# Kernel optimization log

Hardware: AMD Instinct MI355X
Metric: run time of the kernel (lower is better)

## Reference

```python
import jax, jax.numpy as jnp
import numpy as np

B, S, D = 4, 2048, 1024
H, DK, DV = 16, 64, 64
SCALE = 8.0  # scaling_factor = sqrt(dk)


def setup_inputs() -> dict:
    key = jax.random.key(0)
    ks = jax.random.split(key, 9)
    s = 1.0 / np.sqrt(D)
    return {
        "q": jax.random.normal(ks[0], (B, S, D), jnp.float32),
        "k": jax.random.normal(ks[1], (B, S, D), jnp.float32),
        "v": jax.random.normal(ks[2], (B, S, D), jnp.float32),
        "Wq": jax.random.uniform(ks[3], (D, H * DK), jnp.float32, -s, s),
        "bq": jax.random.uniform(ks[4], (H * DK,), jnp.float32, -s, s),
        "Wk": jax.random.uniform(ks[5], (D, H * DK), jnp.float32, -s, s),
        "bk": jax.random.uniform(ks[6], (H * DK,), jnp.float32, -s, s),
        "Wv": jax.random.uniform(ks[7], (D, H * DV), jnp.float32, -s, s),
        "bv": jax.random.uniform(ks[8], (H * DV,), jnp.float32, -s, s),
    }


def reference(q, k, v, Wq, bq, Wk, bk, Wv, bv):
    # Linear projections, then split heads: [B,S,H*d] -> [B,S,H,d]
    qh = (q @ Wq + bq).reshape(B, S, H, DK)
    kh = (k @ Wk + bk).reshape(B, S, H, DK)
    vh = (v @ Wv + bv).reshape(B, S, H, DV)
    # scores: [B,H,Sq,Sk]
    e = jnp.einsum("bqhd,bkhd->bhqk", qh, kh) / SCALE
    attn = jax.nn.softmax(e, axis=-1)
    out = jnp.einsum("bhqk,bkhd->bqhd", attn, vh)  # [B,Sq,H,DV]
    return out.reshape(B, S, H * DV)  # dropout p=0 -> identity
```

## Files before the change

### kernel.cpp

```cpp
#include <hip/hip_runtime.h>
#include <hip/hip_bf16.h>


typedef unsigned short u16;
typedef unsigned int   u32;
typedef short bf16x8 __attribute__((ext_vector_type(8)));
typedef short bf16x4 __attribute__((ext_vector_type(4)));
typedef float f32x4  __attribute__((ext_vector_type(4)));
typedef u32   u32x4  __attribute__((ext_vector_type(4)));

#define S_TOT 2048
#define HD    1024
#define QK_SCALE 0.18033688f

#if __has_builtin(__builtin_amdgcn_exp2f)
#define EXP2(x) __builtin_amdgcn_exp2f(x)
#else
#define EXP2(x) exp2f(x)
#endif

__device__ __forceinline__ u16 f2bf(float f) {
  union { float f; unsigned u; } v; v.f = f;
  unsigned r = v.u + 0x7FFFu + ((v.u >> 16) & 1u);
  return (u16)(r >> 16);
}

__device__ __forceinline__ u32 cvt_pk_bf16(float lo, float hi) {
  u32 r;
  asm("v_cvt_pk_bf16_f32 %0, %1, %2" : "=v"(r) : "v"(lo), "v"(hi));
  return r;
}

__device__ __forceinline__ bf16x4 ds_tr16(unsigned a) {
  bf16x4 d;
  asm volatile("ds_read_b64_tr_b16 %0, %1" : "=v"(d) : "v"(a) : "memory");
  return d;
}

__device__ __forceinline__ void gld16(const u16* g, u16* l) {
  __builtin_amdgcn_global_load_lds(
      (const __attribute__((address_space(1))) u32*)g,
      (__attribute__((address_space(3))) u32*)l, 16, 0, 0);
}

#define LGKM_FENCE() do { asm volatile("s_waitcnt lgkmcnt(0)" ::: "memory"); \
                          __builtin_amdgcn_sched_barrier(0); } while (0)

#define PIPE_BAR(N) do { asm volatile("s_waitcnt vmcnt(" #N ")" ::: "memory"); \
                         __builtin_amdgcn_s_barrier(); \
                         __builtin_amdgcn_sched_barrier(0); } while (0)

__global__ __launch_bounds__(256)
void conv_kernel(const float* __restrict__ x0, const float* __restrict__ x1, const float* __restrict__ x2,
                 const float* __restrict__ w0, const float* __restrict__ w1, const float* __restrict__ w2,
                 u16* __restrict__ Xb, u16* __restrict__ Wt)
{
  const int z = blockIdx.y;
  const int t = threadIdx.x;
  if (blockIdx.x < 1024) {
    const float* X = z == 0 ? x0 : (z == 1 ? x1 : x2);
    u16* Xz = Xb + (size_t)z * 8388608;
    int tid = blockIdx.x * 256 + t;
#pragma unroll
    for (int i = 0; i < 8; ++i) {
      int c = tid + i * 262144;
      int row = c >> 8, k4 = (c & 255) * 4;
      const float4 xv = *(const float4*)&X[(size_t)row * 1024 + k4];
      int p = (k4 & ~31) + 8 * ((k4 & 15) >> 2) + 4 * ((k4 >> 4) & 1);
      p ^= (row & 6) << 2;
      bf16x4 sv = { (short)f2bf(xv.x), (short)f2bf(xv.y), (short)f2bf(xv.z), (short)f2bf(xv.w) };
      *(bf16x4*)&Xz[(size_t)row * 1024 + p] = sv;
    }
  } else {
    const float* W = z == 0 ? w0 : (z == 1 ? w1 : w2);
    u16* Wz = Wt + (size_t)z * 1048576;
    int tid = (blockIdx.x - 1024) * 256 + t;
#pragma unroll
    for (int i = 0; i < 8; ++i) {
      int c = tid + i * 32768;
      int n = c & 1023, k4 = (c >> 10) * 4;
      float wv0 = W[(size_t)(k4 + 0) * 1024 + n];
      float wv1 = W[(size_t)(k4 + 1) * 1024 + n];
      float wv2 = W[(size_t)(k4 + 2) * 1024 + n];
      float wv3 = W[(size_t)(k4 + 3) * 1024 + n];
      int kl = k4 & 31;
      int kp = 8 * ((kl & 15) >> 2) + 4 * ((kl >> 4) & 1);
      int off = ((n >> 7) * 32 + (k4 >> 5)) * 4096 + (n & 127) * 32 + kp;
      bf16x4 sv = { (short)f2bf(wv0), (short)f2bf(wv1), (short)f2bf(wv2), (short)f2bf(wv3) };
      *(bf16x4*)&Wz[off] = sv;
    }
  }
}

__global__ __launch_bounds__(256)
void gemm_kernel(const u16* __restrict__ Xb, const u16* __restrict__ Wt,
                 const float* __restrict__ b0, const float* __restrict__ b1, const float* __restrict__ b2,
                 u16* __restrict__ o0, u16* __restrict__ o1, u16* __restrict__ vT)
{
  int p  = blockIdx.x + 8 * blockIdx.y + 512 * blockIdx.z;
  int wk = (p & 7) * 192 + (p >> 3);
  int nb = wk & 7, mb = (wk >> 3) & 63, z = wk >> 9;

  const u16* Xz = Xb + (size_t)z * 8388608;
  const u16* Wz = Wt + (size_t)z * 1048576;
  const float* BS = z == 0 ? b0 : (z == 1 ? b1 : b2);
  const float  osc = (z == 0) ? QK_SCALE : 1.0f;

  const int t = threadIdx.x;
  const int lane = t & 63, wid = t >> 6;
  const int g = lane >> 4, ln = lane & 15;
  const int mbase = mb * 128, nbase = nb * 128;
  const int xr = (ln & 6) << 2;

  __shared__ __align__(16) u16 Al[3][128 * 32];

  f32x4 acc[4][4];
#pragma unroll
  for (int i = 0; i < 4; ++i)
#pragma unroll
    for (int j = 0; j < 4; ++j) { acc[i][j][0]=0.f; acc[i][j][1]=0.f; acc[i][j][2]=0.f; acc[i][j][3]=0.f; }

  const u16* sa = Xz + (size_t)(mbase + (t >> 2)) * 1024 + (t & 3) * 8;
  u16* alw[3] = { &Al[0][wid * 512], &Al[1][wid * 512], &Al[2][wid * 512] };

  auto stage = [&](int kb, int buf) __attribute__((always_inline)) {
    gld16(sa + kb * 32,               alw[buf]);
    gld16(sa + kb * 32 + 64 * 1024,   alw[buf] + 2048);
  };

  const int whalf = (z < 2) ? (wid & 1) : (wid & 1);
  const u16* wfp = Wz + (size_t)(nb * 32) * 4096
                 + (whalf * 64 + ln) * 32 + g * 8;

  auto loadB = [&](int kb, bf16x8* dst) __attribute__((always_inline)) {
#pragma unroll
    for (int nf = 0; nf < 4; ++nf)
      dst[nf] = *(const bf16x8*)(wfp + (size_t)kb * 4096 + nf * 512);
  };

  bf16x8 bA[4], bB[4];

  stage(0, 0);
  loadB(0, bA);
  stage(1, 1);
  PIPE_BAR(6);

  if (z < 2) {
    const int wm = wid >> 1;
    u16* O = z == 0 ? o0 : o1;

    auto compute = [&](int cur, const bf16x8* bq) __attribute__((always_inline)) {
      bf16x8 af[4];
#pragma unroll
      for (int mf = 0; mf < 4; ++mf)
        af[mf] = *(const bf16x8*)&Al[cur][(wm * 64 + mf * 16 + ln) * 32 + (g * 8 ^ xr)];
      __builtin_amdgcn_s_setprio(1);
#pragma unroll
      for (int mf = 0; mf < 4; ++mf)
#pragma unroll
        for (int nf = 0; nf < 4; ++nf)
          acc[mf][nf] = __builtin_amdgcn_mfma_f32_16x16x32_bf16(af[mf], bq[nf], acc[mf][nf], 0, 0, 0);
      __builtin_amdgcn_s_setprio(0);
    };

    for (int kb = 0; kb < 30; kb += 6) {
      stage(kb + 2, 2); loadB(kb + 1, bB); compute(0, bA); PIPE_BAR(6);
      stage(kb + 3, 0); loadB(kb + 2, bA); compute(1, bB); PIPE_BAR(6);
      stage(kb + 4, 1); loadB(kb + 3, bB); compute(2, bA); PIPE_BAR(6);
      stage(kb + 5, 2); loadB(kb + 4, bA); compute(0, bB); PIPE_BAR(6);
      stage(kb + 6, 0); loadB(kb + 5, bB); compute(1, bA); PIPE_BAR(6);
      stage(kb + 7, 1); loadB(kb + 6, bA); compute(2, bB); PIPE_BAR(6);
    }
    loadB(31, bB); compute(0, bA); PIPE_BAR(0);
    compute(1, bB);

#pragma unroll
    for (int nf = 0; nf < 4; ++nf) {
      int n = nbase + whalf * 64 + nf * 16 + ln;
      float bv = BS[n];
#pragma unroll
      for (int mf = 0; mf < 4; ++mf)
#pragma unroll
        for (int r = 0; r < 4; ++r) {
          int m = mbase + wm * 64 + mf * 16 + 4 * g + r;
          O[(size_t)m * 1024 + n] = f2bf((acc[mf][nf][r] + bv) * osc);
        }
    }
  } else {
    const int wseq = wid >> 1;

    auto compute2 = [&](int cur, const bf16x8* wq) __attribute__((always_inline)) {
      bf16x8 bfx[4];
#pragma unroll
      for (int nf = 0; nf < 4; ++nf)
        bfx[nf] = *(const bf16x8*)&Al[cur][(wseq * 64 + nf * 16 + ln) * 32 + (g * 8 ^ xr)];
      __builtin_amdgcn_s_setprio(1);
#pragma unroll
      for (int mf = 0; mf < 4; ++mf)
#pragma unroll
        for (int nf = 0; nf < 4; ++nf)
          acc[mf][nf] = __builtin_amdgcn_mfma_f32_16x16x32_bf16(wq[mf], bfx[nf], acc[mf][nf], 0, 0, 0);
      __builtin_amdgcn_s_setprio(0);
    };

    for (int kb = 0; kb < 30; kb += 6) {
      stage(kb + 2, 2); loadB(kb + 1, bB); compute2(0, bA); PIPE_BAR(6);
      stage(kb + 3, 0); loadB(kb + 2, bA); compute2(1, bB); PIPE_BAR(6);
      stage(kb + 4, 1); loadB(kb + 3, bB); compute2(2, bA); PIPE_BAR(6);
      stage(kb + 5, 2); loadB(kb + 4, bA); compute2(0, bB); PIPE_BAR(6);
      stage(kb + 6, 0); loadB(kb + 5, bB); compute2(1, bA); PIPE_BAR(6);
      stage(kb + 7, 1); loadB(kb + 6, bA); compute2(2, bB); PIPE_BAR(6);
    }
    loadB(31, bB); compute2(0, bA); PIPE_BAR(0);
    compute2(1, bB);

#pragma unroll
    for (int mf = 0; mf < 4; ++mf)
#pragma unroll
      for (int r = 0; r < 4; ++r) {
        int dvg = nbase + whalf * 64 + mf * 16 + 4 * g + r;
        float bv = BS[dvg];
        int hh = dvg >> 6, dvl = dvg & 63;
#pragma unroll
        for (int nf = 0; nf < 4; ++nf) {
          int m = mbase + wseq * 64 + nf * 16 + ln;
          int bb = m >> 11, ss = m & 2047;
          vT[((size_t)(bb * 16 + hh) * 64 + dvl) * 2048 + ss] = f2bf(acc[mf][nf][r] + bv);
        }
      }
  }
}

__global__ __launch_bounds__(256)
void proj_kernel(const float* __restrict__ x0, const float* __restrict__ x1, const float* __restrict__ x2,
                 const float* __restrict__ w0, const float* __restrict__ w1, const float* __restrict__ w2,
                 const float* __restrict__ b0, const float* __restrict__ b1, const float* __restrict__ b2,
                 u16* __restrict__ o0, u16* __restrict__ o1, u16* __restrict__ vT)
{
  int p  = blockIdx.x + 8 * blockIdx.y + 512 * blockIdx.z;
  int wk = (p & 7) * 192 + (p >> 3);
  int nb = wk & 7, mb = (wk >> 3) & 63, z = wk >> 9;

  const float* X  = z == 0 ? x0 : (z == 1 ? x1 : x2);
  const float* W  = z == 0 ? w0 : (z == 1 ? w1 : w2);
  const float* BS = z == 0 ? b0 : (z == 1 ? b1 : b2);
  const float  osc = (z == 0) ? QK_SCALE : 1.0f;

  const int t = threadIdx.x;
  const int lane = t & 63, wid = t >> 6;
  const int g = lane >> 4, ln = lane & 15;
  const int wm = wid >> 1, wn = wid & 1;
  const int mbase = mb * 128, nbase = nb * 128;

  __shared__ __align__(16) u16 As[128 * 40];
  __shared__ __align__(16) u16 Bs[16 * 272];

  f32x4 acc[4][4];
#pragma unroll
  for (int i = 0; i < 4; ++i)
#pragma unroll
    for (int j = 0; j < 4; ++j) { acc[i][j][0]=0.f; acc[i][j][1]=0.f; acc[i][j][2]=0.f; acc[i][j][3]=0.f; }

  const int arow = t >> 3;
  const int ak0  = (t & 7) * 4;
  const int ap   = 8 * ((ak0 & 15) >> 2) + 4 * (ak0 >> 4);
  const int bkr  = t >> 5;
  const int bnc  = (t & 31) * 4;
  const int bnblk = bnc >> 4, bncl = bnc & 15;

  const unsigned bs_base = (unsigned)(size_t)&Bs[0];

  for (int kb = 0; kb < 32; ++kb) {
    const int kbase = kb * 32;
#pragma unroll
    for (int ps = 0; ps < 4; ++ps) {
      int row = arow + 32 * ps;
      const float4 xv = *(const float4*)&X[(size_t)(mbase + row) * 1024 + kbase + ak0];
      bf16x4 sv = { (short)f2bf(xv.x), (short)f2bf(xv.y), (short)f2bf(xv.z), (short)f2bf(xv.w) };
      *(bf16x4*)&As[row * 40 + ap] = sv;
    }
#pragma unroll
    for (int ps = 0; ps < 4; ++ps) {
      int kr = bkr + 8 * ps;
      const float4 wv = *(const float4*)&W[(size_t)(kbase + kr) * 1024 + nbase + bnc];
      bf16x4 sv = { (short)f2bf(wv.x), (short)f2bf(wv.y), (short)f2bf(wv.z), (short)f2bf(wv.w) };
      *(bf16x4*)&Bs[(bnblk * 2 + (kr >> 4)) * 272 + (kr & 15) * 16 + bncl] = sv;
    }
    __syncthreads();

    bf16x8 af[4];
#pragma unroll
    for (int mf = 0; mf < 4; ++mf)
      af[mf] = *(const bf16x8*)&As[(wm * 64 + mf * 16 + ln) * 40 + g * 8];

    bf16x8 bfv[4];
#pragma unroll
    for (int nf = 0; nf < 4; ++nf) {
      unsigned base = bs_base + (unsigned)(((wn * 4 + nf) * 2) * 544) + lane * 8;
      bf16x4 lo = ds_tr16(base);
      bf16x4 hi = ds_tr16(base + 544);
      bf16x8 bb;
      bb[0]=lo[0]; bb[1]=lo[1]; bb[2]=lo[2]; bb[3]=lo[3];
      bb[4]=hi[0]; bb[5]=hi[1]; bb[6]=hi[2]; bb[7]=hi[3];
      bfv[nf] = bb;
    }
    LGKM_FENCE();
#pragma unroll
    for (int mf = 0; mf < 4; ++mf)
#pragma unroll
      for (int nf = 0; nf < 4; ++nf)
        acc[mf][nf] = __builtin_amdgcn_mfma_f32_16x16x32_bf16(af[mf], bfv[nf], acc[mf][nf], 0, 0, 0);
    __syncthreads();
  }

#pragma unroll
  for (int nf = 0; nf < 4; ++nf) {
    int n = nbase + wn * 64 + nf * 16 + ln;
    float bv = BS[n];
#pragma unroll
    for (int mf = 0; mf < 4; ++mf)
#pragma unroll
      for (int r = 0; r < 4; ++r) {
        int m = mbase + wm * 64 + mf * 16 + 4 * g + r;
        float val = (acc[mf][nf][r] + bv) * osc;
        if (z < 2) {
          u16* O = z == 0 ? o0 : o1;
          O[(size_t)m * 1024 + n] = f2bf(val);
        } else {
          vT[((size_t)((m >> 11) * 16 + (n >> 6)) * 64 + (n & 63)) * 2048 + (m & 2047)] = f2bf(val);
        }
      }
  }
}

__global__ __launch_bounds__(512)
void attn_kernel(const u16* __restrict__ qh, const u16* __restrict__ kh, const u16* __restrict__ vT,
                 float* __restrict__ out)
{
  int p  = blockIdx.x + 8 * blockIdx.y + 128 * blockIdx.z;
  int wk = (p & 7) * 64 + (p >> 3);
  int qt = wk & 7, h = (wk >> 3) & 15, b = wk >> 7;

  const int t = threadIdx.x;
  const int lane = t & 63, wid = t >> 6;
  const int g = lane >> 4, ln = lane & 15;
  const size_t bS = (size_t)b * S_TOT;
  const int qwin = qt * 256 + wid * 32;

  __shared__ __align__(16) u16 Ks[64 * 72];
  __shared__ __align__(16) u16 Vt[64 * 72];

  bf16x8 qf[2][2];
#pragma unroll
  for (int nf = 0; nf < 2; ++nf) {
    const u16* qrow = &qh[(bS + qwin + nf * 16 + ln) * HD + h * 64];
#pragma unroll
    for (int kk = 0; kk < 2; ++kk) {
      bf16x4 lo = *(const bf16x4*)&qrow[kk * 32 + 4 * g];
      bf16x4 hi = *(const bf16x4*)&qrow[kk * 32 + 4 * g + 16];
      bf16x8 qq;
      qq[0]=lo[0]; qq[1]=lo[1]; qq[2]=lo[2]; qq[3]=lo[3];
      qq[4]=hi[0]; qq[5]=hi[1]; qq[6]=hi[2]; qq[7]=hi[3];
      qf[nf][kk] = qq;
    }
  }

  bf16x8 ones;
#pragma unroll
  for (int j = 0; j < 8; ++j) ones[j] = (short)0x3F80;

  f32x4 o[2][4];
#pragma unroll
  for (int i = 0; i < 2; ++i)
#pragma unroll
    for (int j = 0; j < 4; ++j) { o[i][j][0]=0.f; o[i][j][1]=0.f; o[i][j][2]=0.f; o[i][j][3]=0.f; }
  f32x4 o1[2];
  o1[0][0]=0.f; o1[0][1]=0.f; o1[0][2]=0.f; o1[0][3]=0.f;
  o1[1][0]=0.f; o1[1][1]=0.f; o1[1][2]=0.f; o1[1][3]=0.f;

  const int skv = t >> 4;
  const int sd0 = (t & 15) * 4;
  const int kpos = 32 * (sd0 >> 5) + 8 * ((sd0 & 15) >> 2) + 4 * ((sd0 >> 4) & 1);
  u16* ksw[2];
  ksw[0] = &Ks[skv * 72 + kpos];
  ksw[1] = &Ks[(skv + 32) * 72 + kpos];
  const u16* kp = &kh[(bS + skv) * HD + h * 64 + sd0];

  const int vdv  = t >> 3;
  const int vkv8 = (t & 7) * 8;
  const int vp0  = 32 * (vkv8 >> 5) + 8 * ((vkv8 & 15) >> 2) + 4 * ((vkv8 >> 4) & 1);
  const int vkv4 = vkv8 + 4;
  const int vp1  = 32 * (vkv4 >> 5) + 8 * ((vkv4 & 15) >> 2) + 4 * ((vkv4 >> 4) & 1);
  u16* vsw0 = &Vt[vdv * 72 + vp0];
  u16* vsw1 = &Vt[vdv * 72 + vp1];
  const u16* vp = &vT[((size_t)(b * 16 + h) * 64 + vdv) * 2048 + vkv8];

  const size_t KSTEP = (size_t)64 * HD, C32 = (size_t)32 * HD;

  bf16x4 kr[2];
  kr[0] = *(const bf16x4*)kp; kr[1] = *(const bf16x4*)(kp + C32);
  bf16x8 vr = *(const bf16x8*)vp;
  kp += KSTEP; vp += 64;

  for (int it = 0; it < 32; ++it) {
    *(bf16x4*)ksw[0] = kr[0];
    *(bf16x4*)ksw[1] = kr[1];
    bf16x4 vlo = { vr[0], vr[1], vr[2], vr[3] };
    bf16x4 vhi = { vr[4], vr[5], vr[6], vr[7] };
    *(bf16x4*)vsw0 = vlo;
    *(bf16x4*)vsw1 = vhi;
    __syncthreads();

    if (it < 31) {
      kr[0] = *(const bf16x4*)kp; kr[1] = *(const bf16x4*)(kp + C32);
      vr = *(const bf16x8*)vp;
      kp += KSTEP; vp += 64;
    }

#pragma unroll
    for (int s = 0; s < 2; ++s) {
      bf16x8 kf[2][2];
#pragma unroll
      for (int mf = 0; mf < 2; ++mf)
#pragma unroll
        for (int kk = 0; kk < 2; ++kk)
          kf[mf][kk] = *(const bf16x8*)&Ks[(s * 32 + mf * 16 + ln) * 72 + kk * 32 + 8 * g];

      f32x4 sc[2][2];
      __builtin_amdgcn_s_setprio(1);
#pragma unroll
      for (int mf = 0; mf < 2; ++mf)
#pragma unroll
        for (int nf = 0; nf < 2; ++nf) {
          f32x4 a; a[0]=0.f; a[1]=0.f; a[2]=0.f; a[3]=0.f;
#pragma unroll
          for (int kk = 0; kk < 2; ++kk)
            a = __builtin_amdgcn_mfma_f32_16x16x32_bf16(kf[mf][kk], qf[nf][kk], a, 0, 0, 0);
          sc[mf][nf] = a;
        }
      __builtin_amdgcn_s_setprio(0);

      bf16x8 vf[4];
#pragma unroll
      for (int nf = 0; nf < 4; ++nf)
        vf[nf] = *(const bf16x8*)&Vt[(nf * 16 + ln) * 72 + s * 32 + 8 * g];

      bf16x8 pa[2];
#pragma unroll
      for (int nf = 0; nf < 2; ++nf) {
        float pv[2][4];
#pragma unroll
        for (int mf = 0; mf < 2; ++mf)
#pragma unroll
          for (int r = 0; r < 4; ++r)
            pv[mf][r] = EXP2(sc[mf][nf][r]);
        union { u32x4 u; bf16x8 b; } pk;
        pk.u[0] = cvt_pk_bf16(pv[0][0], pv[0][1]);
        pk.u[1] = cvt_pk_bf16(pv[0][2], pv[0][3]);
        pk.u[2] = cvt_pk_bf16(pv[1][0], pv[1][1]);
        pk.u[3] = cvt_pk_bf16(pv[1][2], pv[1][3]);
        pa[nf] = pk.b;
      }

      __builtin_amdgcn_s_setprio(1);
#pragma unroll
      for (int mq = 0; mq < 2; ++mq) {
#pragma unroll
        for (int nf = 0; nf < 4; ++nf)
          o[mq][nf] = __builtin_amdgcn_mfma_f32_16x16x32_bf16(pa[mq], vf[nf], o[mq][nf], 0, 0, 0);
        o1[mq] = __builtin_amdgcn_mfma_f32_16x16x32_bf16(pa[mq], ones, o1[mq], 0, 0, 0);
      }
      __builtin_amdgcn_s_setprio(0);
    }
    __syncthreads();
  }

#pragma unroll
  for (int mq = 0; mq < 2; ++mq)
#pragma unroll
    for (int r = 0; r < 4; ++r) {
      float inv = 1.0f / o1[mq][r];
      int qrow = qwin + mq * 16 + 4 * g + r;
#pragma unroll
      for (int nf = 0; nf < 4; ++nf)
        out[(bS + qrow) * HD + h * 64 + nf * 16 + ln] = o[mq][nf][r] * inv;
    }
}

extern "C" void kernel_launch(void* const* d_in, const int* in_sizes, int n_in,
                              void* d_out, int out_size, void* d_ws, size_t ws_size,
                              hipStream_t stream) {
  const float* q  = (const float*)d_in[0];
  const float* k  = (const float*)d_in[1];
  const float* v  = (const float*)d_in[2];
  const float* Wq = (const float*)d_in[3];
  const float* bq = (const float*)d_in[4];
  const float* Wk = (const float*)d_in[5];
  const float* bk = (const float*)d_in[6];
  const float* Wv = (const float*)d_in[7];
  const float* bv = (const float*)d_in[8];
  float* out = (float*)d_out;

  u16* qh = (u16*)d_ws;
  u16* kh = qh + (size_t)8192 * 1024;
  u16* vT = kh + (size_t)8192 * 1024;

  const size_t XB_OFF = (size_t)3 * 8192 * 1024;
  const size_t WT_OFF = XB_OFF + (size_t)3 * 8192 * 1024;
  const size_t NEED   = (WT_OFF + (size_t)3 * 1024 * 1024) * 2;

  if (ws_size >= NEED) {
    u16* Xb = (u16*)d_ws + XB_OFF;
    u16* Wt = (u16*)d_ws + WT_OFF;
    conv_kernel<<<dim3(1152, 3), 256, 0, stream>>>(q, k, v, Wq, Wk, Wv, Xb, Wt);
    gemm_kernel<<<dim3(8, 64, 3), 256, 0, stream>>>(Xb, Wt, bq, bk, bv, qh, kh, vT);
  } else {
    proj_kernel<<<dim3(8, 64, 3), 256, 0, stream>>>(q, k, v, Wq, Wk, Wv, bq, bk, bv, qh, kh, vT);
  }
  attn_kernel<<<dim3(8, 16, 4), 512, 0, stream>>>(qh, kh, vT, out);
}
```

Before: 168.6 us.

## Enlarge projection GEMM tile to 256 rows with 512 threads and 4-stage LDS pipeline

Result: slower. 183.0 us (+8.5%).

```diff
diff --git a/kernel.cpp b/kernel.cpp
--- a/kernel.cpp
+++ b/kernel.cpp
@@ -92,14 +92,14 @@
   }
 }
 
-__global__ __launch_bounds__(256)
+__global__ __launch_bounds__(512)
 void gemm_kernel(const u16* __restrict__ Xb, const u16* __restrict__ Wt,
                  const float* __restrict__ b0, const float* __restrict__ b1, const float* __restrict__ b2,
                  u16* __restrict__ o0, u16* __restrict__ o1, u16* __restrict__ vT)
 {
-  int p  = blockIdx.x + 8 * blockIdx.y + 512 * blockIdx.z;
-  int wk = (p & 7) * 192 + (p >> 3);
-  int nb = wk & 7, mb = (wk >> 3) & 63, z = wk >> 9;
+  int p  = blockIdx.x + 8 * blockIdx.y + 256 * blockIdx.z;
+  int wk = (p & 7) * 96 + (p >> 3);
+  int nb = wk & 7, mb = (wk >> 3) & 31, z = wk >> 8;
 
   const u16* Xz = Xb + (size_t)z * 8388608;
   const u16* Wz = Wt + (size_t)z * 1048576;
@@ -109,10 +109,12 @@
   const int t = threadIdx.x;
   const int lane = t & 63, wid = t >> 6;
   const int g = lane >> 4, ln = lane & 15;
-  const int mbase = mb * 128, nbase = nb * 128;
+  const int wm = wid >> 1;
+  const int whalf = wid & 1;
+  const int mbase = mb * 256, nbase = nb * 128;
   const int xr = (ln & 6) << 2;
 
-  __shared__ __align__(16) u16 Al[3][128 * 32];
+  __shared__ __align__(16) u16 Al[4][256 * 32];
 
   f32x4 acc[4][4];
 #pragma unroll
@@ -121,17 +123,14 @@
     for (int j = 0; j < 4; ++j) { acc[i][j][0]=0.f; acc[i][j][1]=0.f; acc[i][j][2]=0.f; acc[i][j][3]=0.f; }
 
   const u16* sa = Xz + (size_t)(mbase + (t >> 2)) * 1024 + (t & 3) * 8;
-  u16* alw[3] = { &Al[0][wid * 512], &Al[1][wid * 512], &Al[2][wid * 512] };
+  u16* alw[4] = { &Al[0][wid * 512], &Al[1][wid * 512], &Al[2][wid * 512], &Al[3][wid * 512] };
 
   auto stage = [&](int kb, int buf) __attribute__((always_inline)) {
-    gld16(sa + kb * 32,               alw[buf]);
-    gld16(sa + kb * 32 + 64 * 1024,   alw[buf] + 2048);
+    gld16(sa + kb * 32,                alw[buf]);
+    gld16(sa + kb * 32 + 128 * 1024,   alw[buf] + 4096);
   };
 
-  const int whalf = (z < 2) ? (wid & 1) : (wid & 1);
-  const u16* wfp = Wz + (size_t)(nb * 32) * 4096
-                 + (whalf * 64 + ln) * 32 + g * 8;
-
+  const u16* wfp = Wz + (size_t)(nb * 32) * 4096 + (whalf * 64 + ln) * 32 + g * 8;
   auto loadB = [&](int kb, bf16x8* dst) __attribute__((always_inline)) {
 #pragma unroll
     for (int nf = 0; nf < 4; ++nf)
@@ -141,12 +140,11 @@
   bf16x8 bA[4], bB[4];
 
   stage(0, 0);
+  stage(1, 1);
   loadB(0, bA);
-  stage(1, 1);
-  PIPE_BAR(6);
+  PIPE_BAR(4);
 
   if (z < 2) {
-    const int wm = wid >> 1;
     u16* O = z == 0 ? o0 : o1;
 
     auto compute = [&](int cur, const bf16x8* bq) __attribute__((always_inline)) {
@@ -163,16 +161,16 @@
       __builtin_amdgcn_s_setprio(0);
     };
 
-    for (int kb = 0; kb < 30; kb += 6) {
-      stage(kb + 2, 2); loadB(kb + 1, bB); compute(0, bA); PIPE_BAR(6);
-      stage(kb + 3, 0); loadB(kb + 2, bA); compute(1, bB); PIPE_BAR(6);
-      stage(kb + 4, 1); loadB(kb + 3, bB); compute(2, bA); PIPE_BAR(6);
-      stage(kb + 5, 2); loadB(kb + 4, bA); compute(0, bB); PIPE_BAR(6);
-      stage(kb + 6, 0); loadB(kb + 5, bB); compute(1, bA); PIPE_BAR(6);
-      stage(kb + 7, 1); loadB(kb + 6, bA); compute(2, bB); PIPE_BAR(6);
-    }
-    loadB(31, bB); compute(0, bA); PIPE_BAR(0);
-    compute(1, bB);
+    for (int j = 0; j < 14; j += 2) {
+      int kb = 2 * j;
+      stage(kb + 2, 2); stage(kb + 3, 3); loadB(kb + 1, bB); compute(0, bA);
+      loadB(kb + 2, bA); compute(1, bB); PIPE_BAR(4);
+      stage(kb + 4, 0); stage(kb + 5, 1); loadB(kb + 3, bB); compute(2, bA);
+      loadB(kb + 4, bA); compute(3, bB); PIPE_BAR(4);
+    }
+    stage(30, 2); stage(31, 3); loadB(29, bB); compute(0, bA);
+    loadB(30, bA); compute(1, bB); PIPE_BAR(4);
+    loadB(31, bB); compute(2, bA); compute(3, bB);
 
 #pragma unroll
     for (int nf = 0; nf < 4; ++nf) {
@@ -187,13 +185,11 @@
         }
     }
   } else {
-    const int wseq = wid >> 1;
-
     auto compute2 = [&](int cur, const bf16x8* wq) __attribute__((always_inline)) {
       bf16x8 bfx[4];
 #pragma unroll
       for (int nf = 0; nf < 4; ++nf)
-        bfx[nf] = *(const bf16x8*)&Al[cur][(wseq * 64 + nf * 16 + ln) * 32 + (g * 8 ^ xr)];
+        bfx[nf] = *(const bf16x8*)&Al[cur][(wm * 64 + nf * 16 + ln) * 32 + (g * 8 ^ xr)];
       __builtin_amdgcn_s_setprio(1);
 #pragma unroll
       for (int mf = 0; mf < 4; ++mf)
@@ -203,16 +199,16 @@
       __builtin_amdgcn_s_setprio(0);
     };
 
-    for (int kb = 0; kb < 30; kb += 6) {
-      stage(kb + 2, 2); loadB(kb + 1, bB); compute2(0, bA); PIPE_BAR(6);
-      stage(kb + 3, 0); loadB(kb + 2, bA); compute2(1, bB); PIPE_BAR(6);
-      stage(kb + 4, 1); loadB(kb + 3, bB); compute2(2, bA); PIPE_BAR(6);
-      stage(kb + 5, 2); loadB(kb + 4, bA); compute2(0, bB); PIPE_BAR(6);
-      stage(kb + 6, 0); loadB(kb + 5, bB); compute2(1, bA); PIPE_BAR(6);
-      stage(kb + 7, 1); loadB(kb + 6, bA); compute2(2, bB); PIPE_BAR(6);
-    }
-    loadB(31, bB); compute2(0, bA); PIPE_BAR(0);
-    compute2(1, bB);
+    for (int j = 0; j < 14; j += 2) {
+      int kb = 2 * j;
+      stage(kb + 2, 2); stage(kb + 3, 3); loadB(kb + 1, bB); compute2(0, bA);
+      loadB(kb + 2, bA); compute2(1, bB); PIPE_BAR(4);
+      stage(kb + 4, 0); stage(kb + 5, 1); loadB(kb + 3, bB); compute2(2, bA);
+      loadB(kb + 4, bA); compute2(3, bB); PIPE_BAR(4);
+    }
+    stage(30, 2); stage(31, 3); loadB(29, bB); compute2(0, bA);
+    loadB(30, bA); compute2(1, bB); PIPE_BAR(4);
+    loadB(31, bB); compute2(2, bA); compute2(3, bB);
 
 #pragma unroll
     for (int mf = 0; mf < 4; ++mf)
@@ -223,7 +219,7 @@
         int hh = dvg >> 6, dvl = dvg & 63;
 #pragma unroll
         for (int nf = 0; nf < 4; ++nf) {
-          int m = mbase + wseq * 64 + nf * 16 + ln;
+          int m = mbase + wm * 64 + nf * 16 + ln;
           int bb = m >> 11, ss = m & 2047;
           vT[((size_t)(bb * 16 + hh) * 64 + dvl) * 2048 + ss] = f2bf(acc[mf][nf][r] + bv);
         }
@@ -513,7 +509,7 @@
     u16* Xb = (u16*)d_ws + XB_OFF;
     u16* Wt = (u16*)d_ws + WT_OFF;
     conv_kernel<<<dim3(1152, 3), 256, 0, stream>>>(q, k, v, Wq, Wk, Wv, Xb, Wt);
-    gemm_kernel<<<dim3(8, 64, 3), 256, 0, stream>>>(Xb, Wt, bq, bk, bv, qh, kh, vT);
+    gemm_kernel<<<dim3(8, 32, 3), 512, 0, stream>>>(Xb, Wt, bq, bk, bv, qh, kh, vT);
   } else {
     proj_kernel<<<dim3(8, 64, 3), 256, 0, stream>>>(q, k, v, Wq, Wk, Wv, bq, bk, bv, qh, kh, vT);
   }
```

## Fuse fp32-to-bf16 activation conversion into projection GEMM A-tile staging

Applied to the files above, without the earlier changes.

Measured after the change: 152.9 us. -9.3%, faster.

```diff
diff --git a/kernel.cpp b/kernel.cpp
--- a/kernel.cpp
+++ b/kernel.cpp
@@ -37,63 +37,37 @@
   return d;
 }
 
-__device__ __forceinline__ void gld16(const u16* g, u16* l) {
-  __builtin_amdgcn_global_load_lds(
-      (const __attribute__((address_space(1))) u32*)g,
-      (__attribute__((address_space(3))) u32*)l, 16, 0, 0);
-}
-
 #define LGKM_FENCE() do { asm volatile("s_waitcnt lgkmcnt(0)" ::: "memory"); \
                           __builtin_amdgcn_sched_barrier(0); } while (0)
 
-#define PIPE_BAR(N) do { asm volatile("s_waitcnt vmcnt(" #N ")" ::: "memory"); \
-                         __builtin_amdgcn_s_barrier(); \
-                         __builtin_amdgcn_sched_barrier(0); } while (0)
-
 __global__ __launch_bounds__(256)
-void conv_kernel(const float* __restrict__ x0, const float* __restrict__ x1, const float* __restrict__ x2,
-                 const float* __restrict__ w0, const float* __restrict__ w1, const float* __restrict__ w2,
-                 u16* __restrict__ Xb, u16* __restrict__ Wt)
+void conv_kernel(const float* __restrict__ w0, const float* __restrict__ w1, const float* __restrict__ w2,
+                 u16* __restrict__ Wt)
 {
   const int z = blockIdx.y;
   const int t = threadIdx.x;
-  if (blockIdx.x < 1024) {
-    const float* X = z == 0 ? x0 : (z == 1 ? x1 : x2);
-    u16* Xz = Xb + (size_t)z * 8388608;
-    int tid = blockIdx.x * 256 + t;
-#pragma unroll
-    for (int i = 0; i < 8; ++i) {
-      int c = tid + i * 262144;
-      int row = c >> 8, k4 = (c & 255) * 4;
-      const float4 xv = *(const float4*)&X[(size_t)row * 1024 + k4];
-      int p = (k4 & ~31) + 8 * ((k4 & 15) >> 2) + 4 * ((k4 >> 4) & 1);
-      p ^= (row & 6) << 2;
-      bf16x4 sv = { (short)f2bf(xv.x), (short)f2bf(xv.y), (short)f2bf(xv.z), (short)f2bf(xv.w) };
-      *(bf16x4*)&Xz[(size_t)row * 1024 + p] = sv;
-    }
-  } else {
-    const float* W = z == 0 ? w0 : (z == 1 ? w1 : w2);
-    u16* Wz = Wt + (size_t)z * 1048576;
-    int tid = (blockIdx.x - 1024) * 256 + t;
-#pragma unroll
-    for (int i = 0; i < 8; ++i) {
-      int c = tid + i * 32768;
-      int n = c & 1023, k4 = (c >> 10) * 4;
-      float wv0 = W[(size_t)(k4 + 0) * 1024 + n];
-      float wv1 = W[(size_t)(k4 + 1) * 1024 + n];
-      float wv2 = W[(size_t)(k4 + 2) * 1024 + n];
-      float wv3 = W[(size_t)(k4 + 3) * 1024 + n];
-      int kl = k4 & 31;
-      int kp = 8 * ((kl & 15) >> 2) + 4 * ((kl >> 4) & 1);
-      int off = ((n >> 7) * 32 + (k4 >> 5)) * 4096 + (n & 127) * 32 + kp;
-      bf16x4 sv = { (short)f2bf(wv0), (short)f2bf(wv1), (short)f2bf(wv2), (short)f2bf(wv3) };
-      *(bf16x4*)&Wz[off] = sv;
-    }
+  const float* W = z == 0 ? w0 : (z == 1 ? w1 : w2);
+  u16* Wz = Wt + (size_t)z * 1048576;
+  int tid = blockIdx.x * 256 + t;
+#pragma unroll
+  for (int i = 0; i < 8; ++i) {
+    int c = tid + i * 32768;
+    int n = c & 1023, k4 = (c >> 10) * 4;
+    float wv0 = W[(size_t)(k4 + 0) * 1024 + n];
+    float wv1 = W[(size_t)(k4 + 1) * 1024 + n];
+    float wv2 = W[(size_t)(k4 + 2) * 1024 + n];
+    float wv3 = W[(size_t)(k4 + 3) * 1024 + n];
+    int kl = k4 & 31;
+    int kp = 8 * ((kl & 15) >> 2) + 4 * ((kl >> 4) & 1);
+    int off = ((n >> 7) * 32 + (k4 >> 5)) * 4096 + (n & 127) * 32 + kp;
+    bf16x4 sv = { (short)f2bf(wv0), (short)f2bf(wv1), (short)f2bf(wv2), (short)f2bf(wv3) };
+    *(bf16x4*)&Wz[off] = sv;
   }
 }
 
 __global__ __launch_bounds__(256)
-void gemm_kernel(const u16* __restrict__ Xb, const u16* __restrict__ Wt,
+void gemm_kernel(const float* __restrict__ x0, const float* __restrict__ x1, const float* __restrict__ x2,
+                 const u16* __restrict__ Wt,
                  const float* __restrict__ b0, const float* __restrict__ b1, const float* __restrict__ b2,
                  u16* __restrict__ o0, u16* __restrict__ o1, u16* __restrict__ vT)
 {
@@ -101,8 +75,8 @@
   int wk = (p & 7) * 192 + (p >> 3);
   int nb = wk & 7, mb = (wk >> 3) & 63, z = wk >> 9;
 
-  const u16* Xz = Xb + (size_t)z * 8388608;
-  const u16* Wz = Wt + (size_t)z * 1048576;
+  const float* X  = z == 0 ? x0 : (z == 1 ? x1 : x2);
+  const u16*   Wz = Wt + (size_t)z * 1048576;
   const float* BS = z == 0 ? b0 : (z == 1 ? b1 : b2);
   const float  osc = (z == 0) ? QK_SCALE : 1.0f;
 
@@ -112,7 +86,7 @@
   const int mbase = mb * 128, nbase = nb * 128;
   const int xr = (ln & 6) << 2;
 
-  __shared__ __align__(16) u16 Al[3][128 * 32];
+  __shared__ __align__(16) u16 Al[128 * 32];
 
   f32x4 acc[4][4];
 #pragma unroll
@@ -120,60 +94,81 @@
 #pragma unroll
     for (int j = 0; j < 4; ++j) { acc[i][j][0]=0.f; acc[i][j][1]=0.f; acc[i][j][2]=0.f; acc[i][j][3]=0.f; }
 
-  const u16* sa = Xz + (size_t)(mbase + (t >> 2)) * 1024 + (t & 3) * 8;
-  u16* alw[3] = { &Al[0][wid * 512], &Al[1][wid * 512], &Al[2][wid * 512] };
-
-  auto stage = [&](int kb, int buf) __attribute__((always_inline)) {
-    gld16(sa + kb * 32,               alw[buf]);
-    gld16(sa + kb * 32 + 64 * 1024,   alw[buf] + 2048);
-  };
-
-  const int whalf = (z < 2) ? (wid & 1) : (wid & 1);
-  const u16* wfp = Wz + (size_t)(nb * 32) * 4096
-                 + (whalf * 64 + ln) * 32 + g * 8;
-
+  const int arow = t >> 3;
+  const int ak0  = (t & 7) * 4;
+  const int ap   = 8 * ((ak0 & 15) >> 2) + 4 * ((ak0 >> 4) & 1);
+  const int axr  = (arow & 6) << 2;
+  const int apw  = ap ^ axr;
+  const float* xp = &X[(size_t)(mbase + arow) * 1024 + ak0];
+
+  const int whalf = wid & 1;
+  const u16* wfp = Wz + (size_t)(nb * 32) * 4096 + (whalf * 64 + ln) * 32 + g * 8;
   auto loadB = [&](int kb, bf16x8* dst) __attribute__((always_inline)) {
 #pragma unroll
     for (int nf = 0; nf < 4; ++nf)
       dst[nf] = *(const bf16x8*)(wfp + (size_t)kb * 4096 + nf * 512);
   };
 
+  float4 xrg[4];
   bf16x8 bA[4], bB[4];
 
-  stage(0, 0);
+#pragma unroll
+  for (int ps = 0; ps < 4; ++ps)
+    xrg[ps] = *(const float4*)(xp + (size_t)(32 * ps) * 1024);
+  xp += 32;
   loadB(0, bA);
-  stage(1, 1);
-  PIPE_BAR(6);
-
-  if (z < 2) {
-    const int wm = wid >> 1;
-    u16* O = z == 0 ? o0 : o1;
-
-    auto compute = [&](int cur, const bf16x8* bq) __attribute__((always_inline)) {
-      bf16x8 af[4];
-#pragma unroll
-      for (int mf = 0; mf < 4; ++mf)
-        af[mf] = *(const bf16x8*)&Al[cur][(wm * 64 + mf * 16 + ln) * 32 + (g * 8 ^ xr)];
-      __builtin_amdgcn_s_setprio(1);
+
+  const int wm = wid >> 1;
+
+  auto phase = [&](int kb, const bf16x8* bq, bf16x8* bnext, bool swapped)
+      __attribute__((always_inline)) {
+#pragma unroll
+    for (int ps = 0; ps < 4; ++ps) {
+      int row = arow + 32 * ps;
+      bf16x4 sv = { (short)f2bf(xrg[ps].x), (short)f2bf(xrg[ps].y),
+                    (short)f2bf(xrg[ps].z), (short)f2bf(xrg[ps].w) };
+      *(bf16x4*)&Al[row * 32 + apw] = sv;
+    }
+    __syncthreads();
+
+    if (kb < 31) {
+#pragma unroll
+      for (int ps = 0; ps < 4; ++ps)
+        xrg[ps] = *(const float4*)(xp + (size_t)(32 * ps) * 1024);
+      xp += 32;
+      loadB(kb + 1, bnext);
+    }
+
+    bf16x8 af[4];
+#pragma unroll
+    for (int mf = 0; mf < 4; ++mf)
+      af[mf] = *(const bf16x8*)&Al[(wm * 64 + mf * 16 + ln) * 32 + (g * 8 ^ xr)];
+    __builtin_amdgcn_s_setprio(1);
+    if (!swapped) {
 #pragma unroll
       for (int mf = 0; mf < 4; ++mf)
 #pragma unroll
         for (int nf = 0; nf < 4; ++nf)
           acc[mf][nf] = __builtin_amdgcn_mfma_f32_16x16x32_bf16(af[mf], bq[nf], acc[mf][nf], 0, 0, 0);
-      __builtin_amdgcn_s_setprio(0);
-    };
-
-    for (int kb = 0; kb < 30; kb += 6) {
-      stage(kb + 2, 2); loadB(kb + 1, bB); compute(0, bA); PIPE_BAR(6);
-      stage(kb + 3, 0); loadB(kb + 2, bA); compute(1, bB); PIPE_BAR(6);
-      stage(kb + 4, 1); loadB(kb + 3, bB); compute(2, bA); PIPE_BAR(6);
-      stage(kb + 5, 2); loadB(kb + 4, bA); compute(0, bB); PIPE_BAR(6);
-      stage(kb + 6, 0); loadB(kb + 5, bB); compute(1, bA); PIPE_BAR(6);
-      stage(kb + 7, 1); loadB(kb + 6, bA); compute(2, bB); PIPE_BAR(6);
-    }
-    loadB(31, bB); compute(0, bA); PIPE_BAR(0);
-    compute(1, bB);
-
+    } else {
+#pragma unroll
+      for (int mf = 0; mf < 4; ++mf)
+#pragma unroll
+        for (int nf = 0; nf < 4; ++nf)
+          acc[mf][nf] = __builtin_amdgcn_mfma_f32_16x16x32_bf16(bq[mf], af[nf], acc[mf][nf], 0, 0, 0);
+    }
+    __builtin_amdgcn_s_setprio(0);
+    __syncthreads();
+  };
+
+  const bool swapped = (z == 2);
+  for (int it = 0; it < 16; ++it) {
+    phase(2 * it,     bA, bB, swapped);
+    phase(2 * it + 1, bB, bA, swapped);
+  }
+
+  if (!swapped) {
+    u16* O = z == 0 ? o0 : o1;
 #pragma unroll
     for (int nf = 0; nf < 4; ++nf) {
       int n = nbase + whalf * 64 + nf * 16 + ln;
@@ -187,33 +182,6 @@
         }
     }
   } else {
-    const int wseq = wid >> 1;
-
-    auto compute2 = [&](int cur, const bf16x8* wq) __attribute__((always_inline)) {
-      bf16x8 bfx[4];
-#pragma unroll
-      for (int nf = 0; nf < 4; ++nf)
-        bfx[nf] = *(const bf16x8*)&Al[cur][(wseq * 64 + nf * 16 + ln) * 32 + (g * 8 ^ xr)];
-      __builtin_amdgcn_s_setprio(1);
-#pragma unroll
-      for (int mf = 0; mf < 4; ++mf)
-#pragma unroll
-        for (int nf = 0; nf < 4; ++nf)
-          acc[mf][nf] = __builtin_amdgcn_mfma_f32_16x16x32_bf16(wq[mf], bfx[nf], acc[mf][nf], 0, 0, 0);
-      __builtin_amdgcn_s_setprio(0);
-    };
-
-    for (int kb = 0; kb < 30; kb += 6) {
-      stage(kb + 2, 2); loadB(kb + 1, bB); compute2(0, bA); PIPE_BAR(6);
-      stage(kb + 3, 0); loadB(kb + 2, bA); compute2(1, bB); PIPE_BAR(6);
-      stage(kb + 4, 1); loadB(kb + 3, bB); compute2(2, bA); PIPE_BAR(6);
-      stage(kb + 5, 2); loadB(kb + 4, bA); compute2(0, bB); PIPE_BAR(6);
-      stage(kb + 6, 0); loadB(kb + 5, bB); compute2(1, bA); PIPE_BAR(6);
-      stage(kb + 7, 1); loadB(kb + 6, bA); compute2(2, bB); PIPE_BAR(6);
-    }
-    loadB(31, bB); compute2(0, bA); PIPE_BAR(0);
-    compute2(1, bB);
-
 #pragma unroll
     for (int mf = 0; mf < 4; ++mf)
 #pragma unroll
@@ -223,7 +191,7 @@
         int hh = dvg >> 6, dvl = dvg & 63;
 #pragma unroll
         for (int nf = 0; nf < 4; ++nf) {
-          int m = mbase + wseq * 64 + nf * 16 + ln;
+          int m = mbase + wm * 64 + nf * 16 + ln;
           int bb = m >> 11, ss = m & 2047;
           vT[((size_t)(bb * 16 + hh) * 64 + dvl) * 2048 + ss] = f2bf(acc[mf][nf][r] + bv);
         }
@@ -510,10 +478,9 @@
   const size_t NEED   = (WT_OFF + (size_t)3 * 1024 * 1024) * 2;
 
   if (ws_size >= NEED) {
-    u16* Xb = (u16*)d_ws + XB_OFF;
     u16* Wt = (u16*)d_ws + WT_OFF;
-    conv_kernel<<<dim3(1152, 3), 256, 0, stream>>>(q, k, v, Wq, Wk, Wv, Xb, Wt);
-    gemm_kernel<<<dim3(8, 64, 3), 256, 0, stream>>>(Xb, Wt, bq, bk, bv, qh, kh, vT);
+    conv_kernel<<<dim3(128, 3), 256, 0, stream>>>(Wq, Wk, Wv, Wt);
+    gemm_kernel<<<dim3(8, 64, 3), 256, 0, stream>>>(q, k, v, Wt, bq, bk, bv, qh, kh, vT);
   } else {
     proj_kernel<<<dim3(8, 64, 3), 256, 0, stream>>>(q, k, v, Wq, Wk, Wv, bq, bk, bv, qh, kh, vT);
   }
```
